# Optimization experiments

Hardware: AMD Instinct MI355X
Metric: run time of the kernel (lower is better)

The kernel has to match this reference:

```python
import jax, jax.numpy as jnp
import numpy as np

D_MODEL = 1024
NUM_HEAD = 16
D_K = D_MODEL // NUM_HEAD
B, S = 2, 2048


def setup_inputs() -> dict:
    key = jax.random.key(0)
    ks = jax.random.split(key, 12)
    s = 1.0 / np.sqrt(D_MODEL)
    return {
        "x_q": jax.random.normal(ks[0], (B, S, D_MODEL), jnp.float32),
        "x_k": jax.random.normal(ks[1], (B, S, D_MODEL), jnp.float32),
        "x_v": jax.random.normal(ks[2], (B, S, D_MODEL), jnp.float32),
        "mask": jax.random.randint(ks[3], (B, S, S), 0, 2, jnp.int32),
        "Wq": jax.random.uniform(ks[4], (D_MODEL, D_MODEL), jnp.float32, -s, s),
        "bq": jax.random.uniform(ks[5], (D_MODEL,), jnp.float32, -s, s),
        "Wk": jax.random.uniform(ks[6], (D_MODEL, D_MODEL), jnp.float32, -s, s),
        "bk": jax.random.uniform(ks[7], (D_MODEL,), jnp.float32, -s, s),
        "Wv": jax.random.uniform(ks[8], (D_MODEL, D_MODEL), jnp.float32, -s, s),
        "bv": jax.random.uniform(ks[9], (D_MODEL,), jnp.float32, -s, s),
        "Wo": jax.random.uniform(ks[10], (D_MODEL, D_MODEL), jnp.float32, -s, s),
        "bo": jax.random.uniform(ks[11], (D_MODEL,), jnp.float32, -s, s),
    }


def reference(x_q, x_k, x_v, mask, Wq, bq, Wk, bk, Wv, bv, Wo, bo):
    # projections -> [B, H, S, d_k]
    def proj(x, W, b):
        y = x @ W.T + b
        return y.reshape(B, -1, NUM_HEAD, D_K).transpose(0, 2, 1, 3)

    q = proj(x_q, Wq, bq)
    k = proj(x_k, Wk, bk)
    v = proj(x_v, Wv, bv)
    scale = 1.0 / np.sqrt(D_K).astype(np.float32)
    scores = jnp.einsum("bhqd,bhkd->bhqk", q, k) * scale
    scores = jnp.where(mask[:, None, :, :] == 0, jnp.float32(-1e9), scores)
    p = jax.nn.softmax(scores, axis=-1)  # dropout is identity in eval mode
    attn = jnp.einsum("bhqk,bhkd->bhqd", p, v)
    concat = attn.transpose(0, 2, 1, 3).reshape(B, S, D_MODEL)
    return concat @ Wo.T + bo
```

## Files before the change

kernel.cpp:

```cpp
#include <hip/hip_runtime.h>
#include <cstdint>
#include <cstddef>

#define D_MODELX 1024
#define NUM_HEADX 16
#define D_KX 64
#define BBX 2
#define SSX 2048
#define M_TOK 4096
#define MBYTE (1u << 20)

typedef __attribute__((ext_vector_type(8))) short short8;
typedef __attribute__((ext_vector_type(4))) short short4v;
typedef __attribute__((ext_vector_type(4))) float float4v;
typedef __attribute__((ext_vector_type(16))) float float16v;
typedef __attribute__((ext_vector_type(2))) unsigned uint2v;
typedef __attribute__((ext_vector_type(4))) unsigned uint4v;

__device__ __forceinline__ short f2bf(float f) {
  unsigned u = __builtin_bit_cast(unsigned, f);
  u = u + 0x7FFFu + ((u >> 16) & 1u);
  return (short)(u >> 16);
}

__global__ void mask_bits_kernel(const int* __restrict__ mask, unsigned* __restrict__ mbits) {
  int i = blockIdx.x * blockDim.x + threadIdx.x;
  bool v = mask[i] != 0;
  unsigned long long bal = __ballot(v);
  int lane = threadIdx.x & 63;
  if (lane == 0)       mbits[i >> 5] = (unsigned)bal;
  else if (lane == 32) mbits[i >> 5] = (unsigned)(bal >> 32);
}

__global__ void cvt_w4_kernel(const float* __restrict__ w0, const float* __restrict__ w1,
                              const float* __restrict__ w2, const float* __restrict__ w3,
                              short* __restrict__ o0, short* __restrict__ o1,
                              short* __restrict__ o2, short* __restrict__ o3) {
  int z = blockIdx.y;
  const float* in = (z == 0) ? w0 : (z == 1) ? w1 : (z == 2) ? w2 : w3;
  short* out = (z == 0) ? o0 : (z == 1) ? o1 : (z == 2) ? o2 : o3;
  int i = blockIdx.x * blockDim.x + threadIdx.x;
  float4v v = ((const float4v*)in)[i];
  short4v s;
  s[0] = f2bf(v[0]); s[1] = f2bf(v[1]); s[2] = f2bf(v[2]); s[3] = f2bf(v[3]);
  ((short4v*)out)[i] = s;
}

__global__ void cvt_x3_kernel(const float* __restrict__ x0, const float* __restrict__ x1,
                              const float* __restrict__ x2,
                              short* __restrict__ o0, short* __restrict__ o1,
                              short* __restrict__ o2) {
  int z = blockIdx.y;
  const float* in = (z == 0) ? x0 : (z == 1) ? x1 : x2;
  short* out = (z == 0) ? o0 : (z == 1) ? o1 : o2;
  int i = blockIdx.x * blockDim.x + threadIdx.x;
  float4v v = ((const float4v*)in)[i];
  short4v s;
  s[0] = f2bf(v[0]); s[1] = f2bf(v[1]); s[2] = f2bf(v[2]); s[3] = f2bf(v[3]);
  ((short4v*)out)[i] = s;
}

#define GBK 64

__device__ __forceinline__ void gemm_body(const short* __restrict__ A,
                                          const short* __restrict__ Bw,
                                          const float* __restrict__ bias,
                                          float oscale, void* __restrict__ outp, int mode) {
  __shared__ short lds_a[128 * 64];
  __shared__ short lds_b[128 * 64];
  const int tid = threadIdx.x;
  const int lane = tid & 63;
  const int wid = tid >> 6;
  const int wm = wid >> 1, wn = wid & 1;
  const int bn = blockIdx.y >> 2;
  const int bm = (blockIdx.x << 2) | (blockIdx.y & 3);
  const int l15 = lane & 15, lg = lane >> 4;

  const int s_row = tid >> 3;
  const int s_cB = ((tid & 7) << 4) ^ ((s_row & 7) << 4);
  const short* Abase = A + (size_t)(bm * 128) * 1024 + (s_cB >> 1);
  const short* Bbase = Bw + (size_t)(bn * 128) * 1024 + (s_cB >> 1);

  const int xmask = (l15 & 7) << 4;
  const int a_b0 = (wm * 64 + l15) * 128 + ((lg * 16) ^ xmask);
  const int a_b1 = (wm * 64 + l15) * 128 + ((64 + lg * 16) ^ xmask);
  const int b_b0 = (wn * 64 + l15) * 128 + ((lg * 16) ^ xmask);
  const int b_b1 = (wn * 64 + l15) * 128 + ((64 + lg * 16) ^ xmask);

  float4v acc[4][4];
#pragma unroll
  for (int m = 0; m < 4; ++m)
#pragma unroll
    for (int n = 0; n < 4; ++n) acc[m][n] = (float4v){0.f, 0.f, 0.f, 0.f};

  for (int kt = 0; kt < 1024; kt += GBK) {
#pragma unroll
    for (int it = 0; it < 4; ++it) {
      int row = it * 32 + s_row;
      __builtin_amdgcn_global_load_lds(
          (const uint32_t*)(Abase + (size_t)row * 1024 + kt),
          (uint32_t*)(lds_a + (it * 256 + wid * 64) * 8), 16, 0, 0);
      __builtin_amdgcn_global_load_lds(
          (const uint32_t*)(Bbase + (size_t)row * 1024 + kt),
          (uint32_t*)(lds_b + (it * 256 + wid * 64) * 8), 16, 0, 0);
    }
    __syncthreads();

    short8 af[4][2];
#pragma unroll
    for (int m = 0; m < 4; ++m) {
      af[m][0] = *(const short8*)((const char*)lds_a + a_b0 + m * 2048);
      af[m][1] = *(const short8*)((const char*)lds_a + a_b1 + m * 2048);
    }
#pragma unroll
    for (int n = 0; n < 4; ++n) {
      short8 b0 = *(const short8*)((const char*)lds_b + b_b0 + n * 2048);
      short8 b1 = *(const short8*)((const char*)lds_b + b_b1 + n * 2048);
#pragma unroll
      for (int m = 0; m < 4; ++m) {
        acc[m][n] = __builtin_amdgcn_mfma_f32_16x16x32_bf16(af[m][0], b0, acc[m][n], 0, 0, 0);
        acc[m][n] = __builtin_amdgcn_mfma_f32_16x16x32_bf16(af[m][1], b1, acc[m][n], 0, 0, 0);
      }
    }
    __syncthreads();
  }

#pragma unroll
  for (int n = 0; n < 4; ++n) {
    int col = bn * 128 + wn * 64 + n * 16 + l15;
    float bv = bias[col];
#pragma unroll
    for (int m = 0; m < 4; ++m) {
      if (mode == 2) {
        int base_row = bm * 128 + wm * 64 + m * 16 + lg * 4;
        int bidx = base_row >> 11, s = base_row & 2047;
        int h = col >> 6, d = col & 63;
        short4v sv;
#pragma unroll
        for (int r = 0; r < 4; ++r) sv[r] = f2bf(acc[m][n][r] + bv);
        *(short4v*)&((short*)outp)[(((size_t)(bidx * NUM_HEADX + h)) * D_KX + d) * SSX + s] = sv;
      } else {
#pragma unroll
        for (int r = 0; r < 4; ++r) {
          int row = bm * 128 + wm * 64 + m * 16 + lg * 4 + r;
          float val = (acc[m][n][r] + bv) * oscale;
          if (mode == 0) {
            int bidx = row >> 11, s = row & 2047;
            int h = col >> 6, d = col & 63;
            ((short*)outp)[(((size_t)(bidx * NUM_HEADX + h)) * SSX + s) * D_KX + d] = f2bf(val);
          } else {
            ((float*)outp)[(size_t)row * D_MODELX + col] = val;
          }
        }
      }
    }
  }
}

__global__ __launch_bounds__(256) void gemm_qkv_kernel(
    const short* __restrict__ xq, const short* __restrict__ xk, const short* __restrict__ xv,
    const short* __restrict__ wq, const short* __restrict__ wk, const short* __restrict__ wv,
    const float* __restrict__ bq, const float* __restrict__ bk, const float* __restrict__ bv,
    short* __restrict__ qo, short* __restrict__ ko, short* __restrict__ vo, float qs) {
  int z = blockIdx.z;
  const short* A = (z == 0) ? xq : (z == 1) ? xk : xv;
  const short* W = (z == 0) ? wq : (z == 1) ? wk : wv;
  const float* bi = (z == 0) ? bq : (z == 1) ? bk : bv;
  void* out = (z == 0) ? (void*)qo : (z == 1) ? (void*)ko : (void*)vo;
  float os = (z == 0) ? qs : 1.0f;
  int mode = (z == 2) ? 2 : 0;
  gemm_body(A, W, bi, os, out, mode);
}

__global__ __launch_bounds__(256) void gemm_one_kernel(const short* __restrict__ A,
                                                       const short* __restrict__ W,
                                                       const float* __restrict__ bias,
                                                       float os, void* __restrict__ out, int mode) {
  gemm_body(A, W, bias, os, out, mode);
}

__global__ __launch_bounds__(256, 2) void attn_kernel(const short* __restrict__ q_ws,
                                                      const short* __restrict__ k_ws,
                                                      const short* __restrict__ vT_ws,
                                                      const unsigned* __restrict__ mbits,
                                                      short* __restrict__ attn_ws,
                                                      short* __restrict__ opart,
                                                      float* __restrict__ lpart) {
  __shared__ short k_lds[2][4096];
  __shared__ short vT_lds[2][4096];

  const int tid = threadIdx.x;
  const int lane = tid & 63;
  const int w = tid >> 6;
  const int l31 = lane & 31, hi = lane >> 5;
  const int bid0 = blockIdx.x;
  const int bid = ((bid0 & 7) << 6) | (bid0 >> 3);
  const int qt = bid & 15;
  const int bh = bid >> 4;
  const int b = bh >> 4;
  const int h = bh & 15;
  const int z = blockIdx.z;
  const int nsplit = gridDim.z;
  const int nt = (SSX / 64) / nsplit;
  const int kb0 = z * nt * 64;

  const int qrow = qt * 128 + w * 32;
  const int q = qrow + l31;

  const int xm = (lane & 7) << 4;
  int rd[4];
#pragma unroll
  for (int j = 0; j < 4; ++j) rd[j] = l31 * 128 + ((j * 32 + hi * 16) ^ xm);
  char* kbase = (char*)k_lds;
  char* vbase = (char*)vT_lds;

  const int srow = tid >> 2;
  const int scolS = (tid & 3) * 16;
  const int st0 = srow * 128 + ((scolS * 2) ^ ((srow & 7) << 4));
  const int st1 = srow * 128 + ((scolS * 2 + 16) ^ ((srow & 7) << 4));

  const short* kp = k_ws + (size_t)bh * SSX * D_KX + (size_t)srow * D_KX + scolS;
  const short* vp = vT_ws + (size_t)bh * D_KX * SSX + (size_t)srow * SSX + scolS;

  short8 qf[4];
#pragma unroll
  for (int ds = 0; ds < 4; ++ds)
    qf[ds] = *(const short8*)(q_ws + ((size_t)bh * SSX + q) * D_KX + ds * 16 + hi * 8);

  float16v acc[2];
#pragma unroll
  for (int db = 0; db < 2; ++db)
#pragma unroll
    for (int i = 0; i < 16; ++i) acc[db][i] = 0.f;
  float l_own = 0.f;

  short8 kr0, kr1, vr0, vr1;
  auto loadt = [&](int kb) {
    const short* kq = kp + (size_t)kb * D_KX;
    kr0 = *(const short8*)kq;
    kr1 = *(const short8*)(kq + 8);
    const short* vq = vp + kb;
    vr0 = *(const short8*)vq;
    vr1 = *(const short8*)(vq + 8);
  };
  auto storet = [&](int BUF) {
    *(short8*)(kbase + BUF + st0) = kr0;
    *(short8*)(kbase + BUF + st1) = kr1;
    *(short8*)(vbase + BUF + st0) = vr0;
    *(short8*)(vbase + BUF + st1) = vr1;
  };

  const unsigned* mrow = mbits + ((size_t)b * SSX + q) * (SSX / 32) + (kb0 >> 5);
  unsigned long long mw = *(const unsigned long long*)mrow, mwn = 0;

  loadt(kb0);
  storet(0);
  loadt(kb0 + 64);
  __syncthreads();

  auto step = [&](int t, int CURB, int NXTB) {
    unsigned long long shv = mw >> (hi * 4);

    auto do_kb = [&](const float16v& s, int kb, int CURB_) {
      unsigned wvm = (kb == 0) ? (unsigned)shv : (unsigned)(shv >> 32);
      unsigned cw[8];
      float ls = 0.f;
#pragma unroll
      for (int qd = 0; qd < 4; ++qd) {
        float pv_[4];
#pragma unroll
        for (int r = 0; r < 4; ++r) {
          float e = __builtin_amdgcn_exp2f(s[qd * 4 + r]);
          e = ((wvm >> (qd * 8 + r)) & 1u) ? e : 0.f;
          ls += e;
          pv_[r] = e;
        }
        unsigned u0, u1;
        asm("v_cvt_pk_bf16_f32 %0, %1, %2" : "=v"(u0) : "v"(pv_[0]), "v"(pv_[1]));
        asm("v_cvt_pk_bf16_f32 %0, %1, %2" : "=v"(u1) : "v"(pv_[2]), "v"(pv_[3]));
        cw[qd * 2] = u0;
        cw[qd * 2 + 1] = u1;
      }
      l_own += ls;
#pragma unroll
      for (int g = 0; g < 2; ++g) {
        unsigned a0 = cw[2 * g * 2],     b0 = cw[(2 * g + 1) * 2];
        unsigned a1 = cw[2 * g * 2 + 1], b1 = cw[(2 * g + 1) * 2 + 1];
        asm("v_permlane32_swap_b32 %0, %1" : "+v"(a0), "+v"(b0));
        asm("v_permlane32_swap_b32 %0, %1" : "+v"(a1), "+v"(b1));
        short8 Bf = __builtin_bit_cast(short8, (uint4v){a0, a1, b0, b1});
        __builtin_amdgcn_s_setprio(1);
#pragma unroll
        for (int db = 0; db < 2; ++db) {
          short8 vf = *(const short8*)(vbase + CURB_ + db * 4096 + rd[kb * 2 + g]);
          acc[db] = __builtin_amdgcn_mfma_f32_32x32x16_bf16(vf, Bf, acc[db], 0, 0, 0);
        }
        __builtin_amdgcn_s_setprio(0);
      }
    };

    float16v s0, s1;
#pragma unroll
    for (int i = 0; i < 16; ++i) { s0[i] = 0.f; s1[i] = 0.f; }
    __builtin_amdgcn_s_setprio(1);
#pragma unroll
    for (int ds = 0; ds < 4; ++ds) {
      short8 ka = *(const short8*)(kbase + CURB + rd[ds]);
      short8 kb_ = *(const short8*)(kbase + CURB + 4096 + rd[ds]);
      s0 = __builtin_amdgcn_mfma_f32_32x32x16_bf16(ka, qf[ds], s0, 0, 0, 0);
      s1 = __builtin_amdgcn_mfma_f32_32x32x16_bf16(kb_, qf[ds], s1, 0, 0, 0);
    }
    __builtin_amdgcn_s_setprio(0);

    if (t < nt - 1) storet(NXTB);
    if (t < nt - 2) loadt(kb0 + (t + 2) * 64);
    if (t < nt - 1) mwn = *(const unsigned long long*)(mrow + 2 * (t + 1));

    do_kb(s0, 0, CURB);
    do_kb(s1, 1, CURB);

    asm volatile("s_waitcnt lgkmcnt(0)" ::: "memory");
    __builtin_amdgcn_s_barrier();
    mw = mwn;
  };

  for (int t2 = 0; t2 < nt / 2; ++t2) {
    step(2 * t2, 0, 8192);
    step(2 * t2 + 1, 8192, 0);
  }

  float lp = l_own + __shfl_xor(l_own, 32);
  if (nsplit == 1) {
    float inv = 1.0f / lp;
    size_t ttok = (size_t)b * SSX + q;
#pragma unroll
    for (int db = 0; db < 2; ++db)
#pragma unroll
      for (int qd = 0; qd < 4; ++qd) {
        short4v sv;
#pragma unroll
        for (int r = 0; r < 4; ++r) sv[r] = f2bf(acc[db][qd * 4 + r] * inv);
        *(short4v*)&attn_ws[ttok * D_MODELX + h * 64 + db * 32 + qd * 8 + hi * 4] = sv;
      }
  } else {
    size_t rowp = ((size_t)z * 32 + bh) * SSX + q;
    if (hi == 0) lpart[rowp] = lp;
#pragma unroll
    for (int db = 0; db < 2; ++db)
#pragma unroll
      for (int qd = 0; qd < 4; ++qd) {
        short4v sv;
#pragma unroll
        for (int r = 0; r < 4; ++r) sv[r] = f2bf(acc[db][qd * 4 + r]);
        *(short4v*)&opart[rowp * D_KX + db * 32 + qd * 8 + hi * 4] = sv;
      }
  }
}

__global__ void combine_kernel(const short* __restrict__ opart, const float* __restrict__ lpart,
                               short* __restrict__ attn_ws) {
  int gtid = blockIdx.x * blockDim.x + threadIdx.x;
  int row = gtid >> 3;
  int dc = (gtid & 7) * 8;
  int bh = row >> 11, s = row & 2047;
  int b = bh >> 4, h = bh & 15;
  float inv = 1.0f / (lpart[row] + lpart[row + 32 * SSX]);
  short8 o0 = *(const short8*)&opart[(size_t)row * D_KX + dc];
  short8 o1 = *(const short8*)&opart[((size_t)row + 32 * SSX) * D_KX + dc];
  short8 sv;
#pragma unroll
  for (int j = 0; j < 8; ++j) {
    float f0 = __builtin_bit_cast(float, ((unsigned)(unsigned short)o0[j]) << 16);
    float f1 = __builtin_bit_cast(float, ((unsigned)(unsigned short)o1[j]) << 16);
    sv[j] = f2bf((f0 + f1) * inv);
  }
  *(short8*)&attn_ws[(((size_t)b * SSX + s) * D_MODELX) + h * 64 + dc] = sv;
}

extern "C" void kernel_launch(void* const* d_in, const int* in_sizes, int n_in,
                              void* d_out, int out_size, void* d_ws, size_t ws_size,
                              hipStream_t stream) {
  const float* x_q = (const float*)d_in[0];
  const float* x_k = (const float*)d_in[1];
  const float* x_v = (const float*)d_in[2];
  const int*   mask = (const int*)d_in[3];
  const float* Wq = (const float*)d_in[4];
  const float* bq = (const float*)d_in[5];
  const float* Wk = (const float*)d_in[6];
  const float* bk = (const float*)d_in[7];
  const float* Wv = (const float*)d_in[8];
  const float* bv = (const float*)d_in[9];
  const float* Wo = (const float*)d_in[10];
  const float* bo = (const float*)d_in[11];

  const float QSCALE = 0.125f * 1.44269504089f;

  char* ws = (char*)d_ws;
  short* q_ws  = (short*)(ws + 0 * MBYTE);
  short* k_ws  = (short*)(ws + 8 * MBYTE);
  short* vT_ws = (short*)(ws + 16 * MBYTE);

  dim3 ggrid(D_MODELX / 128, M_TOK / 128);

  if (ws_size >= (size_t)56 * MBYTE) {
    short* wq_bf = (short*)(ws + 24 * MBYTE);
    short* wk_bf = (short*)(ws + 26 * MBYTE);
    short* wv_bf = (short*)(ws + 28 * MBYTE);
    short* wo_bf = (short*)(ws + 30 * MBYTE);
    short* xq_bf = (short*)(ws + 32 * MBYTE);
    short* xk_bf = (short*)(ws + 40 * MBYTE);
    short* xv_bf = (short*)(ws + 48 * MBYTE);
    unsigned* mbits = (unsigned*)(ws + 24 * MBYTE);
    float* lpart    = (float*)(ws + 25 * MBYTE);
    short* attn_ws  = (short*)(ws + 32 * MBYTE);
    short* opart    = (short*)(ws + 40 * MBYTE);

    cvt_w4_kernel<<<dim3(1024, 4), 256, 0, stream>>>(Wq, Wk, Wv, Wo, wq_bf, wk_bf, wv_bf, wo_bf);
    cvt_x3_kernel<<<dim3(4096, 3), 256, 0, stream>>>(x_q, x_k, x_v, xq_bf, xk_bf, xv_bf);

    dim3 qkvgrid(D_MODELX / 128, M_TOK / 128, 3);
    gemm_qkv_kernel<<<qkvgrid, 256, 0, stream>>>(xq_bf, xk_bf, xv_bf, wq_bf, wk_bf, wv_bf,
                                                 bq, bk, bv, q_ws, k_ws, vT_ws, QSCALE);

    mask_bits_kernel<<<(BBX * SSX * SSX) / 256, 256, 0, stream>>>(mask, mbits);

    dim3 agrid(BBX * NUM_HEADX * (SSX / 128), 1, 2);
    attn_kernel<<<agrid, 256, 0, stream>>>(q_ws, k_ws, vT_ws, mbits, attn_ws, opart, lpart);
    combine_kernel<<<2048, 256, 0, stream>>>(opart, lpart, attn_ws);

    gemm_one_kernel<<<ggrid, 256, 0, stream>>>(attn_ws, wo_bf, bo, 1.0f, d_out, 1);
  } else {
    unsigned* mbits = (unsigned*)(ws + 24 * MBYTE);
    short* w_bf = (short*)(ws + 25 * MBYTE);
    short* x_bf = (short*)(ws + 27 * MBYTE);
    short* attn_ws = (short*)(ws + 27 * MBYTE);

    mask_bits_kernel<<<(BBX * SSX * SSX) / 256, 256, 0, stream>>>(mask, mbits);

    cvt_w4_kernel<<<dim3(1024, 1), 256, 0, stream>>>(Wq, Wq, Wq, Wq, w_bf, w_bf, w_bf, w_bf);
    cvt_x3_kernel<<<dim3(4096, 1), 256, 0, stream>>>(x_q, x_q, x_q, x_bf, x_bf, x_bf);
    gemm_one_kernel<<<ggrid, 256, 0, stream>>>(x_bf, w_bf, bq, QSCALE, q_ws, 0);

    cvt_w4_kernel<<<dim3(1024, 1), 256, 0, stream>>>(Wk, Wk, Wk, Wk, w_bf, w_bf, w_bf, w_bf);
    cvt_x3_kernel<<<dim3(4096, 1), 256, 0, stream>>>(x_k, x_k, x_k, x_bf, x_bf, x_bf);
    gemm_one_kernel<<<ggrid, 256, 0, stream>>>(x_bf, w_bf, bk, 1.0f, k_ws, 0);

    cvt_w4_kernel<<<dim3(1024, 1), 256, 0, stream>>>(Wv, Wv, Wv, Wv, w_bf, w_bf, w_bf, w_bf);
    cvt_x3_kernel<<<dim3(4096, 1), 256, 0, stream>>>(x_v, x_v, x_v, x_bf, x_bf, x_bf);
    gemm_one_kernel<<<ggrid, 256, 0, stream>>>(x_bf, w_bf, bv, 1.0f, vT_ws, 2);

    dim3 agrid(BBX * NUM_HEADX * (SSX / 128), 1, 1);
    attn_kernel<<<agrid, 256, 0, stream>>>(q_ws, k_ws, vT_ws, mbits, attn_ws, nullptr, nullptr);

    cvt_w4_kernel<<<dim3(1024, 1), 256, 0, stream>>>(Wo, Wo, Wo, Wo, w_bf, w_bf, w_bf, w_bf);
    gemm_one_kernel<<<ggrid, 256, 0, stream>>>(attn_ws, w_bf, bo, 1.0f, d_out, 1);
  }
}
```

Measured before the change: 158.0 us.

## Double-buffer GEMM LDS tiles with BK=32 and merge conversion launches

The projection GEMM body now uses two LDS buffers of 128x32 tiles. It prefetches the next K-slice with global_load_lds while computing the current one, so each step needs one barrier instead of two, and the LDS swizzle is rewritten for the narrower tile. The weight and activation bf16 conversions are merged into a single prep kernel launch, and the fallback path uses a grid-stride cvt kernel. The prep kernel also carries a mask-packing branch, but the launch grid never reaches it, so mask_bits_kernel still runs separately. The smaller K tile doubles the number of loop iterations and their per-step overhead.

```diff
diff --git a/kernel.cpp b/kernel.cpp
--- a/kernel.cpp
+++ b/kernel.cpp
@@ -23,6 +23,48 @@
   return (short)(u >> 16);
 }
 
+__global__ void prep_kernel(const float* __restrict__ w0, const float* __restrict__ w1,
+                            const float* __restrict__ w2, const float* __restrict__ w3,
+                            short* __restrict__ o0, short* __restrict__ o1,
+                            short* __restrict__ o2, short* __restrict__ o3,
+                            const float* __restrict__ x0, const float* __restrict__ x1,
+                            const float* __restrict__ x2,
+                            short* __restrict__ xo0, short* __restrict__ xo1,
+                            short* __restrict__ xo2,
+                            const int* __restrict__ mask, unsigned* __restrict__ mbits) {
+  int y = blockIdx.y;
+  int i0 = blockIdx.x * blockDim.x + threadIdx.x;
+  if (y < 4) {
+    const float* in = (y == 0) ? w0 : (y == 1) ? w1 : (y == 2) ? w2 : w3;
+    short* out = (y == 0) ? o0 : (y == 1) ? o1 : (y == 2) ? o2 : o3;
+    float4v v = ((const float4v*)in)[i0];
+    short4v s;
+    s[0] = f2bf(v[0]); s[1] = f2bf(v[1]); s[2] = f2bf(v[2]); s[3] = f2bf(v[3]);
+    ((short4v*)out)[i0] = s;
+  } else if (y < 7) {
+    const float* in = (y == 4) ? x0 : (y == 5) ? x1 : x2;
+    short* out = (y == 4) ? xo0 : (y == 5) ? xo1 : xo2;
+#pragma unroll
+    for (int k = 0; k < 4; ++k) {
+      int i = i0 + k * 262144;
+      float4v v = ((const float4v*)in)[i];
+      short4v s;
+      s[0] = f2bf(v[0]); s[1] = f2bf(v[1]); s[2] = f2bf(v[2]); s[3] = f2bf(v[3]);
+      ((short4v*)out)[i] = s;
+    }
+  } else {
+    int lane = threadIdx.x & 63;
+#pragma unroll
+    for (int k = 0; k < 32; ++k) {
+      int i = i0 + k * 262144;
+      bool v = mask[i] != 0;
+      unsigned long long bal = __ballot(v);
+      if (lane == 0)       mbits[i >> 5] = (unsigned)bal;
+      else if (lane == 32) mbits[i >> 5] = (unsigned)(bal >> 32);
+    }
+  }
+}
+
 __global__ void mask_bits_kernel(const int* __restrict__ mask, unsigned* __restrict__ mbits) {
   int i = blockIdx.x * blockDim.x + threadIdx.x;
   bool v = mask[i] != 0;
@@ -32,42 +74,25 @@
   else if (lane == 32) mbits[i >> 5] = (unsigned)(bal >> 32);
 }
 
-__global__ void cvt_w4_kernel(const float* __restrict__ w0, const float* __restrict__ w1,
-                              const float* __restrict__ w2, const float* __restrict__ w3,
-                              short* __restrict__ o0, short* __restrict__ o1,
-                              short* __restrict__ o2, short* __restrict__ o3) {
-  int z = blockIdx.y;
-  const float* in = (z == 0) ? w0 : (z == 1) ? w1 : (z == 2) ? w2 : w3;
-  short* out = (z == 0) ? o0 : (z == 1) ? o1 : (z == 2) ? o2 : o3;
+__global__ void cvt_kernel(const float* __restrict__ in, short* __restrict__ out, int n4) {
   int i = blockIdx.x * blockDim.x + threadIdx.x;
-  float4v v = ((const float4v*)in)[i];
-  short4v s;
-  s[0] = f2bf(v[0]); s[1] = f2bf(v[1]); s[2] = f2bf(v[2]); s[3] = f2bf(v[3]);
-  ((short4v*)out)[i] = s;
-}
-
-__global__ void cvt_x3_kernel(const float* __restrict__ x0, const float* __restrict__ x1,
-                              const float* __restrict__ x2,
-                              short* __restrict__ o0, short* __restrict__ o1,
-                              short* __restrict__ o2) {
-  int z = blockIdx.y;
-  const float* in = (z == 0) ? x0 : (z == 1) ? x1 : x2;
-  short* out = (z == 0) ? o0 : (z == 1) ? o1 : o2;
-  int i = blockIdx.x * blockDim.x + threadIdx.x;
-  float4v v = ((const float4v*)in)[i];
-  short4v s;
-  s[0] = f2bf(v[0]); s[1] = f2bf(v[1]); s[2] = f2bf(v[2]); s[3] = f2bf(v[3]);
-  ((short4v*)out)[i] = s;
-}
-
-#define GBK 64
+  int stride = gridDim.x * blockDim.x;
+  for (; i < n4; i += stride) {
+    float4v v = ((const float4v*)in)[i];
+    short4v s;
+    s[0] = f2bf(v[0]); s[1] = f2bf(v[1]); s[2] = f2bf(v[2]); s[3] = f2bf(v[3]);
+    ((short4v*)out)[i] = s;
+  }
+}
+
+#define GBK 32
 
 __device__ __forceinline__ void gemm_body(const short* __restrict__ A,
                                           const short* __restrict__ Bw,
                                           const float* __restrict__ bias,
                                           float oscale, void* __restrict__ outp, int mode) {
-  __shared__ short lds_a[128 * 64];
-  __shared__ short lds_b[128 * 64];
+  __shared__ short lds_a[2][128 * 32];
+  __shared__ short lds_b[2][128 * 32];
   const int tid = threadIdx.x;
   const int lane = tid & 63;
   const int wid = tid >> 6;
@@ -76,16 +101,32 @@
   const int bm = (blockIdx.x << 2) | (blockIdx.y & 3);
   const int l15 = lane & 15, lg = lane >> 4;
 
-  const int s_row = tid >> 3;
-  const int s_cB = ((tid & 7) << 4) ^ ((s_row & 7) << 4);
-  const short* Abase = A + (size_t)(bm * 128) * 1024 + (s_cB >> 1);
-  const short* Bbase = Bw + (size_t)(bn * 128) * 1024 + (s_cB >> 1);
-
-  const int xmask = (l15 & 7) << 4;
-  const int a_b0 = (wm * 64 + l15) * 128 + ((lg * 16) ^ xmask);
-  const int a_b1 = (wm * 64 + l15) * 128 + ((64 + lg * 16) ^ xmask);
-  const int b_b0 = (wn * 64 + l15) * 128 + ((lg * 16) ^ xmask);
-  const int b_b1 = (wn * 64 + l15) * 128 + ((64 + lg * 16) ^ xmask);
+  const int row0 = tid >> 2, sub = tid & 3;
+  const int row1 = 64 + row0;
+  const int sc0 = ((sub * 16) ^ (((row0 >> 1) & 3) << 4)) >> 1;
+  const int sc1 = ((sub * 16) ^ (((row1 >> 1) & 3) << 4)) >> 1;
+  const short* Asrc0 = A + (size_t)(bm * 128 + row0) * 1024 + sc0;
+  const short* Asrc1 = A + (size_t)(bm * 128 + row1) * 1024 + sc1;
+  const short* Bsrc0 = Bw + (size_t)(bn * 128 + row0) * 1024 + sc0;
+  const short* Bsrc1 = Bw + (size_t)(bn * 128 + row1) * 1024 + sc1;
+
+  const int xm = ((l15 >> 1) & 3) << 4;
+  const int rb = l15 * 64 + ((lg * 16) ^ xm);
+  char* abase = (char*)lds_a;
+  char* bbase = (char*)lds_b;
+  const int a_off = rb + wm * 4096;
+  const int b_off = rb + wn * 4096;
+
+  auto stage = [&](int kt, int BUF) {
+    __builtin_amdgcn_global_load_lds((const uint32_t*)(Asrc0 + kt),
+        (uint32_t*)(abase + BUF + tid * 16), 16, 0, 0);
+    __builtin_amdgcn_global_load_lds((const uint32_t*)(Asrc1 + kt),
+        (uint32_t*)(abase + BUF + 4096 + tid * 16), 16, 0, 0);
+    __builtin_amdgcn_global_load_lds((const uint32_t*)(Bsrc0 + kt),
+        (uint32_t*)(bbase + BUF + tid * 16), 16, 0, 0);
+    __builtin_amdgcn_global_load_lds((const uint32_t*)(Bsrc1 + kt),
+        (uint32_t*)(bbase + BUF + 4096 + tid * 16), 16, 0, 0);
+  };
 
   float4v acc[4][4];
 #pragma unroll
@@ -93,36 +134,28 @@
 #pragma unroll
     for (int n = 0; n < 4; ++n) acc[m][n] = (float4v){0.f, 0.f, 0.f, 0.f};
 
-  for (int kt = 0; kt < 1024; kt += GBK) {
-#pragma unroll
-    for (int it = 0; it < 4; ++it) {
-      int row = it * 32 + s_row;
-      __builtin_amdgcn_global_load_lds(
-          (const uint32_t*)(Abase + (size_t)row * 1024 + kt),
-          (uint32_t*)(lds_a + (it * 256 + wid * 64) * 8), 16, 0, 0);
-      __builtin_amdgcn_global_load_lds(
-          (const uint32_t*)(Bbase + (size_t)row * 1024 + kt),
-          (uint32_t*)(lds_b + (it * 256 + wid * 64) * 8), 16, 0, 0);
+  stage(0, 0);
+  __syncthreads();
+
+  auto step = [&](int t, int CUR, int NXT) {
+    if (t < 31) stage((t + 1) * GBK, NXT);
+    short8 af[4];
+#pragma unroll
+    for (int m = 0; m < 4; ++m)
+      af[m] = *(const short8*)(abase + CUR + a_off + m * 1024);
+#pragma unroll
+    for (int n = 0; n < 4; ++n) {
+      short8 bf = *(const short8*)(bbase + CUR + b_off + n * 1024);
+#pragma unroll
+      for (int m = 0; m < 4; ++m)
+        acc[m][n] = __builtin_amdgcn_mfma_f32_16x16x32_bf16(af[m], bf, acc[m][n], 0, 0, 0);
     }
     __syncthreads();
-
-    short8 af[4][2];
-#pragma unroll
-    for (int m = 0; m < 4; ++m) {
-      af[m][0] = *(const short8*)((const char*)lds_a + a_b0 + m * 2048);
-      af[m][1] = *(const short8*)((const char*)lds_a + a_b1 + m * 2048);
-    }
-#pragma unroll
-    for (int n = 0; n < 4; ++n) {
-      short8 b0 = *(const short8*)((const char*)lds_b + b_b0 + n * 2048);
-      short8 b1 = *(const short8*)((const char*)lds_b + b_b1 + n * 2048);
-#pragma unroll
-      for (int m = 0; m < 4; ++m) {
-        acc[m][n] = __builtin_amdgcn_mfma_f32_16x16x32_bf16(af[m][0], b0, acc[m][n], 0, 0, 0);
-        acc[m][n] = __builtin_amdgcn_mfma_f32_16x16x32_bf16(af[m][1], b1, acc[m][n], 0, 0, 0);
-      }
-    }
-    __syncthreads();
+  };
+
+  for (int t2 = 0; t2 < 16; ++t2) {
+    step(2 * t2, 0, 8192);
+    step(2 * t2 + 1, 8192, 0);
   }
 
 #pragma unroll
@@ -415,8 +448,9 @@
     short* attn_ws  = (short*)(ws + 32 * MBYTE);
     short* opart    = (short*)(ws + 40 * MBYTE);
 
-    cvt_w4_kernel<<<dim3(1024, 4), 256, 0, stream>>>(Wq, Wk, Wv, Wo, wq_bf, wk_bf, wv_bf, wo_bf);
-    cvt_x3_kernel<<<dim3(4096, 3), 256, 0, stream>>>(x_q, x_k, x_v, xq_bf, xk_bf, xv_bf);
+    prep_kernel<<<dim3(1024, 7), 256, 0, stream>>>(Wq, Wk, Wv, Wo, wq_bf, wk_bf, wv_bf, wo_bf,
+                                                   x_q, x_k, x_v, xq_bf, xk_bf, xv_bf,
+                                                   mask, (unsigned*)ws );
 
     dim3 qkvgrid(D_MODELX / 128, M_TOK / 128, 3);
     gemm_qkv_kernel<<<qkvgrid, 256, 0, stream>>>(xq_bf, xk_bf, xv_bf, wq_bf, wk_bf, wv_bf,
@@ -434,25 +468,27 @@
     short* w_bf = (short*)(ws + 25 * MBYTE);
     short* x_bf = (short*)(ws + 27 * MBYTE);
     short* attn_ws = (short*)(ws + 27 * MBYTE);
+    const int NX4 = M_TOK * D_MODELX / 4;
+    const int NW4 = D_MODELX * D_MODELX / 4;
 
     mask_bits_kernel<<<(BBX * SSX * SSX) / 256, 256, 0, stream>>>(mask, mbits);
 
-    cvt_w4_kernel<<<dim3(1024, 1), 256, 0, stream>>>(Wq, Wq, Wq, Wq, w_bf, w_bf, w_bf, w_bf);
-    cvt_x3_kernel<<<dim3(4096, 1), 256, 0, stream>>>(x_q, x_q, x_q, x_bf, x_bf, x_bf);
+    cvt_kernel<<<1024, 256, 0, stream>>>(Wq, w_bf, NW4);
+    cvt_kernel<<<2048, 256, 0, stream>>>(x_q, x_bf, NX4);
     gemm_one_kernel<<<ggrid, 256, 0, stream>>>(x_bf, w_bf, bq, QSCALE, q_ws, 0);
 
-    cvt_w4_kernel<<<dim3(1024, 1), 256, 0, stream>>>(Wk, Wk, Wk, Wk, w_bf, w_bf, w_bf, w_bf);
-    cvt_x3_kernel<<<dim3(4096, 1), 256, 0, stream>>>(x_k, x_k, x_k, x_bf, x_bf, x_bf);
+    cvt_kernel<<<1024, 256, 0, stream>>>(Wk, w_bf, NW4);
+    cvt_kernel<<<2048, 256, 0, stream>>>(x_k, x_bf, NX4);
     gemm_one_kernel<<<ggrid, 256, 0, stream>>>(x_bf, w_bf, bk, 1.0f, k_ws, 0);
 
-    cvt_w4_kernel<<<dim3(1024, 1), 256, 0, stream>>>(Wv, Wv, Wv, Wv, w_bf, w_bf, w_bf, w_bf);
-    cvt_x3_kernel<<<dim3(4096, 1), 256, 0, stream>>>(x_v, x_v, x_v, x_bf, x_bf, x_bf);
+    cvt_kernel<<<1024, 256, 0, stream>>>(Wv, w_bf, NW4);
+    cvt_kernel<<<2048, 256, 0, stream>>>(x_v, x_bf, NX4);
     gemm_one_kernel<<<ggrid, 256, 0, stream>>>(x_bf, w_bf, bv, 1.0f, vT_ws, 2);
 
     dim3 agrid(BBX * NUM_HEADX * (SSX / 128), 1, 1);
     attn_kernel<<<agrid, 256, 0, stream>>>(q_ws, k_ws, vT_ws, mbits, attn_ws, nullptr, nullptr);
 
-    cvt_w4_kernel<<<dim3(1024, 1), 256, 0, stream>>>(Wo, Wo, Wo, Wo, w_bf, w_bf, w_bf, w_bf);
+    cvt_kernel<<<1024, 256, 0, stream>>>(Wo, w_bf, NW4);
     gemm_one_kernel<<<ggrid, 256, 0, stream>>>(attn_ws, w_bf, bo, 1.0f, d_out, 1);
   }
 }
```

After: 159.6 us. About the same (+1.0%).
